# Kernel tuning notes

Measured on AMD Instinct MI355X. Metric: run time of the kernel, lower is better.

The kernel has to match this reference:

```python
import jax, jax.numpy as jnp
import numpy as np

N_NODES = 50000
N_EDGES = 625000
HIDDEN = 128
N_TYPES = 4


def setup_inputs() -> dict:
    key = jax.random.key(0)
    ks = jax.random.split(key, 10)
    s = 1.0 / np.sqrt(HIDDEN)
    return {
        "node_states": jax.random.normal(ks[0], (N_NODES, HIDDEN), dtype=jnp.float32),
        "edge_index": jax.random.randint(ks[1], (2, N_EDGES), 0, N_NODES, dtype=jnp.int64),
        "edge_type": jax.random.randint(ks[2], (N_EDGES,), 0, N_TYPES, dtype=jnp.int64),
        # per-edge-type Linear(hidden, hidden): weight [T, d, d] (torch: y = x @ W.T + b)
        "edge_W": jax.random.uniform(ks[3], (N_TYPES, HIDDEN, HIDDEN), jnp.float32, -s, s),
        "edge_b": jax.random.uniform(ks[4], (N_TYPES, HIDDEN), jnp.float32, -s, s),
        # GRUCell params (torch layout: [3d, d] for r|z|n gates)
        "w_ih": jax.random.uniform(ks[5], (3 * HIDDEN, HIDDEN), jnp.float32, -s, s),
        "w_hh": jax.random.uniform(ks[6], (3 * HIDDEN, HIDDEN), jnp.float32, -s, s),
        "b_ih": jax.random.uniform(ks[7], (3 * HIDDEN,), jnp.float32, -s, s),
        "b_hh": jax.random.uniform(ks[8], (3 * HIDDEN,), jnp.float32, -s, s),
    }


def reference(node_states, edge_index, edge_type, edge_W, edge_b, w_ih, w_hh, b_ih, b_hh):
    num_nodes = node_states.shape[0]
    src, dst = edge_index[0], edge_index[1]
    x_src = node_states[src]  # [E, d] gather of source states

    # per-edge-type linear; small fixed loop over edge types, masked accumulate
    msgs = jnp.zeros_like(x_src)
    for t in range(edge_W.shape[0]):
        m_t = x_src @ edge_W[t].T + edge_b[t]  # [E, d]
        msgs = msgs + jnp.where((edge_type == t)[:, None], m_t, 0.0)

    # scatter-sum messages into destination nodes
    agg = jax.ops.segment_sum(msgs, dst, num_segments=num_nodes)  # [N, d]

    # GRUCell(agg, node_states) — torch semantics
    gi = agg @ w_ih.T + b_ih          # [N, 3d]
    gh = node_states @ w_hh.T + b_hh  # [N, 3d]
    i_r, i_z, i_n = jnp.split(gi, 3, axis=1)
    h_r, h_z, h_n = jnp.split(gh, 3, axis=1)
    r = jax.nn.sigmoid(i_r + h_r)
    z = jax.nn.sigmoid(i_z + h_z)
    n = jnp.tanh(i_n + r * h_n)
    return (1.0 - z) * n + z * node_states
```

## Files before the change

kernel.cpp:

```cpp
#include <hip/hip_runtime.h>


typedef __attribute__((ext_vector_type(8))) short short8;
typedef __attribute__((ext_vector_type(4))) float floatx4;

#define HID 128
#define NTY 4

__device__ __forceinline__ unsigned short f2bf(float f) {
    unsigned int u = __float_as_uint(f);
    unsigned int r = (u + 0x7fffu + ((u >> 16) & 1u)) >> 16;
    return (unsigned short)r;
}
__device__ __forceinline__ float bf2f(unsigned int lo16) {
    return __uint_as_float(lo16 << 16);
}
__device__ __forceinline__ float frcp(float x) { return __builtin_amdgcn_rcpf(x); }


__global__ void prep_kernel(const float* __restrict__ h, unsigned short* __restrict__ hbf,
                            const float* __restrict__ W, unsigned short* __restrict__ Wc,
                            const float* __restrict__ w_ih, const float* __restrict__ w_hh,
                            unsigned short* __restrict__ Wg, float* __restrict__ bias4,
                            const float* __restrict__ b_ih, const float* __restrict__ b_hh,
                            int* __restrict__ deg4, int total4, int nb_cvt, int N4) {
    int b = blockIdx.x, tt = threadIdx.x;
    if (b < nb_cvt) {
        int i = b * 256 + tt;
        if (i < total4) {
            float4 v = ((const float4*)h)[i];
            uint2 o;
            o.x = (unsigned int)f2bf(v.x) | ((unsigned int)f2bf(v.y) << 16);
            o.y = (unsigned int)f2bf(v.z) | ((unsigned int)f2bf(v.w) << 16);
            ((uint2*)hbf)[i] = o;
        }
    } else if (b < nb_cvt + 256) {
        int idx = (b - nb_cvt) * 256 + tt;
        int j = idx >> 9, rem = idx & 511;
        int t = rem >> 7, k = rem & 127;
        Wc[idx] = f2bf(W[(t * HID + j) * HID + k]);
    } else if (b < nb_cvt + 768) {
        int idx = (b - nb_cvt - 256) * 256 + tt;
        int row = idx >> 8, k = idx & 255;
        int j = row >> 2, g = row & 3;
        float v = 0.0f;
        if (g == 0) v = (k < 128) ? w_ih[j * 128 + k]         : w_hh[j * 128 + (k - 128)];
        else if (g == 1) v = (k < 128) ? w_ih[(128 + j) * 128 + k] : w_hh[(128 + j) * 128 + (k - 128)];
        else if (g == 2) v = (k < 128) ? w_ih[(256 + j) * 128 + k] : 0.0f;
        else             v = (k < 128) ? 0.0f : w_hh[(256 + j) * 128 + (k - 128)];
        Wg[idx] = f2bf(v);
    } else if (b == nb_cvt + 768) {
        if (tt < 128) {
            float4 v;
            v.x = b_ih[tt] + b_hh[tt];
            v.y = b_ih[128 + tt] + b_hh[128 + tt];
            v.z = b_ih[256 + tt];
            v.w = b_hh[256 + tt];
            ((float4*)bias4)[tt] = v;
        }
    } else {
        int i = (b - nb_cvt - 769) * 256 + tt;
        if (i < N4) deg4[i] = 0;
    }
}


__global__ void hist4_kernel(const int* __restrict__ dst, const int* __restrict__ ety,
                             int* __restrict__ deg4, int E) {
    int e = blockIdx.x * blockDim.x + threadIdx.x;
    if (e < E) atomicAdd(&deg4[dst[e] * 4 + ety[e]], 1);
}

__global__ void scan_blocks4_kernel(const int* __restrict__ deg, int* __restrict__ rowptr,
                                    int* __restrict__ blocksum, int N4) {
    __shared__ int s[256];
    int t = threadIdx.x;
    int base = blockIdx.x * 1024 + t * 4;
    int v0 = 0, v1 = 0, v2 = 0, v3 = 0;
    if (base + 3 < N4) {
        v0 = deg[base]; v1 = deg[base + 1]; v2 = deg[base + 2]; v3 = deg[base + 3];
    } else {
        if (base < N4) v0 = deg[base];
        if (base + 1 < N4) v1 = deg[base + 1];
        if (base + 2 < N4) v2 = deg[base + 2];
    }
    int sum = v0 + v1 + v2 + v3;
    s[t] = sum;
    __syncthreads();
#pragma unroll
    for (int off = 1; off < 256; off <<= 1) {
        int x = (t >= off) ? s[t - off] : 0;
        __syncthreads();
        s[t] += x;
        __syncthreads();
    }
    int ex = s[t] - sum;
    if (base < N4) rowptr[base] = ex;
    if (base + 1 < N4) rowptr[base + 1] = ex + v0;
    if (base + 2 < N4) rowptr[base + 2] = ex + v0 + v1;
    if (base + 3 < N4) rowptr[base + 3] = ex + v0 + v1 + v2;
    if (t == 255) blocksum[blockIdx.x] = s[255];
}

__global__ void scan_top_kernel(const int* __restrict__ blocksum, int* __restrict__ blockoff, int nb) {
    __shared__ int s[256];
    int t = threadIdx.x;
    int v = (t < nb) ? blocksum[t] : 0;
    s[t] = v;
    __syncthreads();
#pragma unroll
    for (int off = 1; off < 256; off <<= 1) {
        int x = (t >= off) ? s[t - off] : 0;
        __syncthreads();
        s[t] += x;
        __syncthreads();
    }
    if (t < nb) blockoff[t] = s[t] - v;
}

__global__ void finalize4_kernel(int* __restrict__ rowptr, const int* __restrict__ blockoff,
                                 int* __restrict__ cursor, int N4, int E) {
    int i = blockIdx.x * blockDim.x + threadIdx.x;
    if (i >= N4) return;
    int r = rowptr[i] + blockoff[i >> 10];
    rowptr[i] = r;
    cursor[i] = r;
    if (i == 0) rowptr[N4] = E;
}

__global__ void fill4_kernel(const int* __restrict__ src, const int* __restrict__ dst,
                             const int* __restrict__ ety, int* __restrict__ cursor,
                             int* __restrict__ csr, int E) {
    int e = blockIdx.x * blockDim.x + threadIdx.x;
    if (e >= E) return;
    int pos = atomicAdd(&cursor[dst[e] * 4 + ety[e]], 1);
    csr[pos] = src[e];
}


__global__ void gather_s_kernel(const int* __restrict__ rowptr4, const int* __restrict__ csr,
                                const unsigned int* __restrict__ hbu,
                                float4* __restrict__ cnt4, unsigned int* __restrict__ Su, int N) {
    int w = blockIdx.x * (blockDim.x >> 6) + (threadIdx.x >> 6);
    if (w >= N) return;
    int lane = threadIdx.x & 63;
    int b0 = __builtin_amdgcn_readfirstlane(rowptr4[w * 4]);
    int b1 = __builtin_amdgcn_readfirstlane(rowptr4[w * 4 + 1]);
    int b2 = __builtin_amdgcn_readfirstlane(rowptr4[w * 4 + 2]);
    int b3 = __builtin_amdgcn_readfirstlane(rowptr4[w * 4 + 3]);
    int b4 = __builtin_amdgcn_readfirstlane(rowptr4[w * 4 + 4]);

    float s0 = 0.f, s1 = 0.f;
    float sn0[3], sn1[3];

    int e = b0;
    while (e + 8 <= b4) {
        int p[8];
        unsigned int u[8];
#pragma unroll
        for (int i = 0; i < 8; ++i) p[i] = csr[e + i];
#pragma unroll
        for (int i = 0; i < 8; ++i) u[i] = hbu[(size_t)p[i] * 64 + lane];
#pragma unroll
        for (int i = 0; i < 8; ++i) {
            int idx = e + i;
            if (idx == b1) { sn0[0] = s0; sn1[0] = s1; }
            if (idx == b2) { sn0[1] = s0; sn1[1] = s1; }
            if (idx == b3) { sn0[2] = s0; sn1[2] = s1; }
            s0 += bf2f(u[i] & 0xffffu);
            s1 += bf2f(u[i] >> 16);
        }
        e += 8;
    }
    {
        int rem = b4 - e;
        int p[7];
        unsigned int u[7];
#pragma unroll
        for (int i = 0; i < 7; ++i) if (i < rem) p[i] = csr[e + i];
#pragma unroll
        for (int i = 0; i < 7; ++i) if (i < rem) u[i] = hbu[(size_t)p[i] * 64 + lane];
#pragma unroll
        for (int i = 0; i < 7; ++i) {
            if (i < rem) {
                int idx = e + i;
                if (idx == b1) { sn0[0] = s0; sn1[0] = s1; }
                if (idx == b2) { sn0[1] = s0; sn1[1] = s1; }
                if (idx == b3) { sn0[2] = s0; sn1[2] = s1; }
                s0 += bf2f(u[i] & 0xffffu);
                s1 += bf2f(u[i] >> 16);
            }
        }
    }
    if (b1 == b4) { sn0[0] = s0; sn1[0] = s1; }
    if (b2 == b4) { sn0[1] = s0; sn1[1] = s1; }
    if (b3 == b4) { sn0[2] = s0; sn1[2] = s1; }

    size_t base = (size_t)w * 256 + lane;
    float a0, a1, p0 = 0.f, p1 = 0.f;
#pragma unroll
    for (int t = 0; t < 4; ++t) {
        float c0 = (t < 3) ? sn0[t] : s0;
        float c1 = (t < 3) ? sn1[t] : s1;
        a0 = c0 - p0; a1 = c1 - p1;
        p0 = c0; p1 = c1;
        Su[base + t * 64] = (unsigned int)f2bf(a0) | ((unsigned int)f2bf(a1) << 16);
    }
    if (lane == 0)
        cnt4[w] = make_float4((float)(b1 - b0), (float)(b2 - b1),
                              (float)(b3 - b2), (float)(b4 - b3));
}


__global__ __launch_bounds__(512, 4) void agg_gru(const unsigned short* __restrict__ S,
                                                  const unsigned short* __restrict__ Wc,
                                                  const unsigned short* __restrict__ Wg,
                                                  const unsigned short* __restrict__ hbf,
                                                  const float4* __restrict__ cnt4,
                                                  const float* __restrict__ eb,
                                                  const float4* __restrict__ bias4,
                                                  float* __restrict__ out, int M) {
    __shared__ __align__(16) unsigned short Sreg[64 * 128];
    __shared__ __align__(16) unsigned short Wreg[128 * 128];
    __shared__ __align__(16) unsigned short Xagg[64 * 128];
    float* OutsF = (float*)Wreg;

    const int tid = threadIdx.x;
    const int m0 = blockIdx.x * 64;
    const int lane = tid & 63, w = tid >> 6;
    const int lm = lane & 15, quad = lane >> 4;
    const uint4 Z = {0u, 0u, 0u, 0u};

    const int sr = tid >> 4;
    const int sg = tid & 15;

    floatx4 accA[4];
#pragma unroll
    for (int a = 0; a < 4; ++a) accA[a] = (floatx4){0.f, 0.f, 0.f, 0.f};

#pragma unroll 1
    for (int c = 0; c < 4; ++c) {
        {
            int gA = m0 + sr, gB = m0 + 32 + sr;
            uint4 vA = (gA < M) ? *(const uint4*)(S + (size_t)gA * 512 + c * 128 + sg * 8) : Z;
            uint4 vB = (gB < M) ? *(const uint4*)(S + (size_t)gB * 512 + c * 128 + sg * 8) : Z;
            *(uint4*)&Sreg[sr * 128 + ((sg ^ (sr & 7)) << 3)] = vA;
            *(uint4*)&Sreg[(32 + sr) * 128 + ((sg ^ (sr & 7)) << 3)] = vB;
        }
#pragma unroll
        for (int p = 0; p < 4; ++p) {
            int j = p * 32 + sr;
            uint4 v = *(const uint4*)(Wc + (size_t)j * 512 + c * 128 + sg * 8);
            *(uint4*)&Wreg[j * 128 + ((sg ^ (j & 7)) << 3)] = v;
        }
        __syncthreads();
#pragma unroll
        for (int ss = 0; ss < 4; ++ss) {
            int g = ss * 4 + quad;
            short8 bw = *(const short8*)&Wreg[(w * 16 + lm) * 128 + ((g ^ (lm & 7)) << 3)];
#pragma unroll
            for (int mi = 0; mi < 4; ++mi) {
                short8 av = *(const short8*)&Sreg[(mi * 16 + lm) * 128 + ((g ^ (lm & 7)) << 3)];
                accA[mi] = __builtin_amdgcn_mfma_f32_16x16x32_bf16(av, bw, accA[mi], 0, 0, 0);
            }
        }
        __syncthreads();
    }

    {
        int j = w * 16 + lm;
        float e0 = eb[j], e1 = eb[HID + j], e2 = eb[2 * HID + j], e3 = eb[3 * HID + j];
        int jg = j >> 3, jr = j & 7;
#pragma unroll
        for (int mi = 0; mi < 4; ++mi) {
#pragma unroll
            for (int r = 0; r < 4; ++r) {
                int nl = mi * 16 + quad * 4 + r;
                int gn = m0 + nl;
                if (gn >= M) gn = M - 1;
                float4 c4 = cnt4[gn];
                float v = accA[mi][r] + c4.x * e0 + c4.y * e1 + c4.z * e2 + c4.w * e3;
                Xagg[nl * 128 + ((jg ^ (nl & 7)) << 3) + jr] = f2bf(v);
            }
        }
    }
    __syncthreads();

    {
        int gA = m0 + sr, gB = m0 + 32 + sr;
        uint4 vA = (gA < M) ? *(const uint4*)(hbf + (size_t)gA * HID + sg * 8) : Z;
        uint4 vB = (gB < M) ? *(const uint4*)(hbf + (size_t)gB * HID + sg * 8) : Z;
        *(uint4*)&Sreg[sr * 128 + ((sg ^ (sr & 7)) << 3)] = vA;
        *(uint4*)&Sreg[(32 + sr) * 128 + ((sg ^ (sr & 7)) << 3)] = vB;
    }

    float fin[4][4];

#pragma unroll 1
    for (int gc = 0; gc < 4; ++gc) {
        floatx4 accB[4];
#pragma unroll
        for (int a = 0; a < 4; ++a) accB[a] = (floatx4){0.f, 0.f, 0.f, 0.f};

#pragma unroll 1
        for (int kc = 0; kc < 2; ++kc) {
#pragma unroll
            for (int p = 0; p < 4; ++p) {
                int rr = p * 32 + sr;
                int grow = gc * 128 + rr;
                uint4 v = *(const uint4*)(Wg + (size_t)grow * 256 + kc * 128 + sg * 8);
                *(uint4*)&Wreg[rr * 128 + ((sg ^ (rr & 7)) << 3)] = v;
            }
            __syncthreads();
#pragma unroll
            for (int ss = 0; ss < 4; ++ss) {
                int g = ss * 4 + quad;
                short8 af = *(const short8*)&Wreg[(w * 16 + lm) * 128 + ((g ^ (lm & 7)) << 3)];
#pragma unroll
                for (int ni = 0; ni < 4; ++ni) {
                    const unsigned short* bsrc = kc ? Sreg : Xagg;
                    short8 bfr = *(const short8*)&bsrc[(ni * 16 + lm) * 128 + ((g ^ (lm & 7)) << 3)];
                    accB[ni] = __builtin_amdgcn_mfma_f32_16x16x32_bf16(af, bfr, accB[ni], 0, 0, 0);
                }
            }
            __syncthreads();
        }

        {
            int j = gc * 32 + w * 4 + quad;
            float4 bb = bias4[j];
            int jg = j >> 3, jr = j & 7;
#pragma unroll
            for (int ni = 0; ni < 4; ++ni) {
                int nl = ni * 16 + lm;
                float g0 = accB[ni][0], g1 = accB[ni][1];
                float g2 = accB[ni][2], g3 = accB[ni][3];
                float rr = frcp(1.f + __expf(-(g0 + bb.x)));
                float zz = frcp(1.f + __expf(-(g1 + bb.y)));
                float aa = g2 + bb.z + rr * (g3 + bb.w);
                float nn = 1.f - 2.f * frcp(1.f + __expf(2.f * aa));
                float hv = bf2f((unsigned int)Sreg[nl * 128 + ((jg ^ (nl & 7)) << 3) + jr]);
                fin[gc][ni] = nn + zz * (hv - nn);
            }
        }
    }
    __syncthreads();

#pragma unroll
    for (int gc = 0; gc < 4; ++gc) {
        int j = gc * 32 + w * 4 + quad;
        int gq = j >> 2, jr = j & 3;
#pragma unroll
        for (int ni = 0; ni < 4; ++ni) {
            int nl = ni * 16 + lm;
            OutsF[nl * 128 + ((gq ^ (nl & 7)) << 2) + jr] = fin[gc][ni];
        }
    }
    __syncthreads();

    {
        int row = tid >> 3;
        int cb = (tid & 7) * 16;
        int node = m0 + row;
        if (node < M) {
            float* dstp = out + (size_t)node * HID + cb;
#pragma unroll
            for (int i = 0; i < 4; ++i) {
                int gq = (cb >> 2) + i;
                *(float4*)(dstp + i * 4) = *(const float4*)&OutsF[row * 128 + ((gq ^ (row & 7)) << 2)];
            }
        }
    }
}


extern "C" void kernel_launch(void* const* d_in, const int* in_sizes, int n_in,
                              void* d_out, int out_size, void* d_ws, size_t ws_size,
                              hipStream_t stream) {
    const float* node_states = (const float*)d_in[0];
    const int*   edge_index  = (const int*)d_in[1];
    const int*   edge_type   = (const int*)d_in[2];
    const float* edge_W      = (const float*)d_in[3];
    const float* edge_b      = (const float*)d_in[4];
    const float* w_ih        = (const float*)d_in[5];
    const float* w_hh        = (const float*)d_in[6];
    const float* b_ih        = (const float*)d_in[7];
    const float* b_hh        = (const float*)d_in[8];

    const int M = in_sizes[0] / HID;
    const int E = in_sizes[1] / 2;
    const int N4 = M * 4;
    const int* src = edge_index;
    const int* dst = edge_index + E;

    char* ws = (char*)d_ws;
    size_t off = 0;
    unsigned short* hbf   = (unsigned short*)(ws + off); off += (size_t)M * HID * 2;
    float*          bias4 = (float*)(ws + off);          off += (size_t)128 * 4 * 4;
    unsigned short* S     = (unsigned short*)(ws + off); off += (size_t)M * 512 * 2;
    unsigned short* Wcat  = (unsigned short*)(ws + off); off += (size_t)128 * 512 * 2;
    unsigned short* Wgru  = (unsigned short*)(ws + off); off += (size_t)512 * 256 * 2;
    float*          cnt4  = (float*)(ws + off);          off += (size_t)M * 4 * 4;
    int* deg4     = (int*)(ws + off); off += (size_t)N4 * 4;
    int* rowptr4  = (int*)(ws + off); off += (size_t)(N4 + 1) * 4;
    int* cursor4  = (int*)(ws + off); off += (size_t)N4 * 4;
    int* blocksum = (int*)(ws + off); off += 256 * 4;
    int* blockoff = (int*)(ws + off); off += 256 * 4;
    int* csr      = (int*)(ws + off); off += (size_t)E * 4;

    const int total4 = M * HID / 4;
    const int nb_cvt = (total4 + 255) / 256;
    const int nb_zero = (N4 + 255) / 256;
    const int nb_scan = (N4 + 1023) / 1024;

    prep_kernel<<<nb_cvt + 769 + nb_zero, 256, 0, stream>>>(
        node_states, hbf, edge_W, Wcat, w_ih, w_hh, Wgru, bias4, b_ih, b_hh,
        deg4, total4, nb_cvt, N4);

    hist4_kernel<<<(E + 255) / 256, 256, 0, stream>>>(dst, edge_type, deg4, E);
    scan_blocks4_kernel<<<nb_scan, 256, 0, stream>>>(deg4, rowptr4, blocksum, N4);
    scan_top_kernel<<<1, 256, 0, stream>>>(blocksum, blockoff, nb_scan);
    finalize4_kernel<<<(N4 + 255) / 256, 256, 0, stream>>>(rowptr4, blockoff, cursor4, N4, E);
    fill4_kernel<<<(E + 255) / 256, 256, 0, stream>>>(src, dst, edge_type, cursor4, csr, E);

    gather_s_kernel<<<(M + 3) / 4, 256, 0, stream>>>(rowptr4, csr, (const unsigned int*)hbf,
                                                     (float4*)cnt4, (unsigned int*)S, M);

    agg_gru<<<(M + 63) / 64, 512, 0, stream>>>(S, Wcat, Wgru, hbf, (const float4*)cnt4,
                                               edge_b, (const float4*)bias4, (float*)d_out, M);
}
```

Measured before the change: 244.6 us.

## Fuse CSR build into one cooperative kernel; double-buffer agg_gru weight tiles

New measurement: 819.8 us. 235% more time.

```diff
diff --git a/kernel.cpp b/kernel.cpp
--- a/kernel.cpp
+++ b/kernel.cpp
@@ -1,4 +1,7 @@
 #include <hip/hip_runtime.h>
+#include <hip/hip_cooperative_groups.h>
+
+namespace cg = cooperative_groups;
 
 
 typedef __attribute__((ext_vector_type(8))) short short8;
@@ -23,7 +26,7 @@
                             const float* __restrict__ w_ih, const float* __restrict__ w_hh,
                             unsigned short* __restrict__ Wg, float* __restrict__ bias4,
                             const float* __restrict__ b_ih, const float* __restrict__ b_hh,
-                            int* __restrict__ deg4, int total4, int nb_cvt, int N4) {
+                            int total4, int nb_cvt) {
     int b = blockIdx.x, tt = threadIdx.x;
     if (b < nb_cvt) {
         int i = b * 256 + tt;
@@ -49,7 +52,7 @@
         else if (g == 2) v = (k < 128) ? w_ih[(256 + j) * 128 + k] : 0.0f;
         else             v = (k < 128) ? 0.0f : w_hh[(256 + j) * 128 + (k - 128)];
         Wg[idx] = f2bf(v);
-    } else if (b == nb_cvt + 768) {
+    } else {
         if (tt < 128) {
             float4 v;
             v.x = b_ih[tt] + b_hh[tt];
@@ -58,83 +61,88 @@
             v.w = b_hh[256 + tt];
             ((float4*)bias4)[tt] = v;
         }
-    } else {
-        int i = (b - nb_cvt - 769) * 256 + tt;
-        if (i < N4) deg4[i] = 0;
-    }
-}
-
-
-__global__ void hist4_kernel(const int* __restrict__ dst, const int* __restrict__ ety,
-                             int* __restrict__ deg4, int E) {
-    int e = blockIdx.x * blockDim.x + threadIdx.x;
-    if (e < E) atomicAdd(&deg4[dst[e] * 4 + ety[e]], 1);
-}
-
-__global__ void scan_blocks4_kernel(const int* __restrict__ deg, int* __restrict__ rowptr,
-                                    int* __restrict__ blocksum, int N4) {
+    }
+}
+
+
+struct CsrArgs {
+    const int* src; const int* dst; const int* ety;
+    int* deg4; int* rowptr4; int* cursor4; int* blocksum; int* blockoff; int* csr;
+    int E, N4;
+};
+
+__global__ __launch_bounds__(256, 4) void csr_build(CsrArgs a) {
+    cg::grid_group grid = cg::this_grid();
     __shared__ int s[256];
-    int t = threadIdx.x;
-    int base = blockIdx.x * 1024 + t * 4;
-    int v0 = 0, v1 = 0, v2 = 0, v3 = 0;
-    if (base + 3 < N4) {
-        v0 = deg[base]; v1 = deg[base + 1]; v2 = deg[base + 2]; v3 = deg[base + 3];
-    } else {
-        if (base < N4) v0 = deg[base];
-        if (base + 1 < N4) v1 = deg[base + 1];
-        if (base + 2 < N4) v2 = deg[base + 2];
-    }
-    int sum = v0 + v1 + v2 + v3;
-    s[t] = sum;
-    __syncthreads();
-#pragma unroll
-    for (int off = 1; off < 256; off <<= 1) {
-        int x = (t >= off) ? s[t - off] : 0;
+    const int t = threadIdx.x;
+    const int gtid = blockIdx.x * 256 + t;
+    const int nth = gridDim.x * 256;
+
+    for (int i = gtid; i < a.N4; i += nth) a.deg4[i] = 0;
+    grid.sync();
+
+    for (int e = gtid; e < a.E; e += nth)
+        atomicAdd(&a.deg4[a.dst[e] * 4 + a.ety[e]], 1);
+    grid.sync();
+
+    const int nbscan = (a.N4 + 1023) >> 10;
+    for (int vb = blockIdx.x; vb < nbscan; vb += gridDim.x) {
+        int base = vb * 1024 + t * 4;
+        int v0 = 0, v1 = 0, v2 = 0, v3 = 0;
+        if (base + 3 < a.N4) {
+            v0 = a.deg4[base]; v1 = a.deg4[base + 1]; v2 = a.deg4[base + 2]; v3 = a.deg4[base + 3];
+        } else {
+            if (base < a.N4) v0 = a.deg4[base];
+            if (base + 1 < a.N4) v1 = a.deg4[base + 1];
+            if (base + 2 < a.N4) v2 = a.deg4[base + 2];
+        }
+        int sum = v0 + v1 + v2 + v3;
+        s[t] = sum;
         __syncthreads();
-        s[t] += x;
+#pragma unroll
+        for (int off = 1; off < 256; off <<= 1) {
+            int x = (t >= off) ? s[t - off] : 0;
+            __syncthreads();
+            s[t] += x;
+            __syncthreads();
+        }
+        int ex = s[t] - sum;
+        if (base < a.N4) a.rowptr4[base] = ex;
+        if (base + 1 < a.N4) a.rowptr4[base + 1] = ex + v0;
+        if (base + 2 < a.N4) a.rowptr4[base + 2] = ex + v0 + v1;
+        if (base + 3 < a.N4) a.rowptr4[base + 3] = ex + v0 + v1 + v2;
+        if (t == 255) a.blocksum[vb] = s[255];
         __syncthreads();
     }
-    int ex = s[t] - sum;
-    if (base < N4) rowptr[base] = ex;
-    if (base + 1 < N4) rowptr[base + 1] = ex + v0;
-    if (base + 2 < N4) rowptr[base + 2] = ex + v0 + v1;
-    if (base + 3 < N4) rowptr[base + 3] = ex + v0 + v1 + v2;
-    if (t == 255) blocksum[blockIdx.x] = s[255];
-}
-
-__global__ void scan_top_kernel(const int* __restrict__ blocksum, int* __restrict__ blockoff, int nb) {
-    __shared__ int s[256];
-    int t = threadIdx.x;
-    int v = (t < nb) ? blocksum[t] : 0;
-    s[t] = v;
-    __syncthreads();
-#pragma unroll
-    for (int off = 1; off < 256; off <<= 1) {
-        int x = (t >= off) ? s[t - off] : 0;
+    grid.sync();
+
+    if (blockIdx.x == 0) {
+        int v = (t < nbscan) ? a.blocksum[t] : 0;
+        s[t] = v;
         __syncthreads();
-        s[t] += x;
-        __syncthreads();
-    }
-    if (t < nb) blockoff[t] = s[t] - v;
-}
-
-__global__ void finalize4_kernel(int* __restrict__ rowptr, const int* __restrict__ blockoff,
-                                 int* __restrict__ cursor, int N4, int E) {
-    int i = blockIdx.x * blockDim.x + threadIdx.x;
-    if (i >= N4) return;
-    int r = rowptr[i] + blockoff[i >> 10];
-    rowptr[i] = r;
-    cursor[i] = r;
-    if (i == 0) rowptr[N4] = E;
-}
-
-__global__ void fill4_kernel(const int* __restrict__ src, const int* __restrict__ dst,
-                             const int* __restrict__ ety, int* __restrict__ cursor,
-                             int* __restrict__ csr, int E) {
-    int e = blockIdx.x * blockDim.x + threadIdx.x;
-    if (e >= E) return;
-    int pos = atomicAdd(&cursor[dst[e] * 4 + ety[e]], 1);
-    csr[pos] = src[e];
+#pragma unroll
+        for (int off = 1; off < 256; off <<= 1) {
+            int x = (t >= off) ? s[t - off] : 0;
+            __syncthreads();
+            s[t] += x;
+            __syncthreads();
+        }
+        if (t < nbscan) a.blockoff[t] = s[t] - v;
+    }
+    grid.sync();
+
+    for (int i = gtid; i < a.N4; i += nth) {
+        int r = a.rowptr4[i] + a.blockoff[i >> 10];
+        a.rowptr4[i] = r;
+        a.cursor4[i] = r;
+    }
+    if (gtid == 0) a.rowptr4[a.N4] = a.E;
+    grid.sync();
+
+    for (int e = gtid; e < a.E; e += nth) {
+        int pos = atomicAdd(&a.cursor4[a.dst[e] * 4 + a.ety[e]], 1);
+        a.csr[pos] = a.src[e];
+    }
 }
 
 
@@ -220,51 +228,55 @@
                                                   const float* __restrict__ eb,
                                                   const float4* __restrict__ bias4,
                                                   float* __restrict__ out, int M) {
-    __shared__ __align__(16) unsigned short Sreg[64 * 128];
-    __shared__ __align__(16) unsigned short Wreg[128 * 128];
-    __shared__ __align__(16) unsigned short Xagg[64 * 128];
-    float* OutsF = (float*)Wreg;
+    __shared__ __align__(16) unsigned char smem[65536];
+    unsigned short* SdB = (unsigned short*)smem;
+    unsigned short* WdB = (unsigned short*)(smem + 16384);
+    unsigned short* Xag = (unsigned short*)(smem + 49152);
+    unsigned short* Hbt = (unsigned short*)smem;
+    float* OutsF = (float*)smem;
 
     const int tid = threadIdx.x;
     const int m0 = blockIdx.x * 64;
     const int lane = tid & 63, w = tid >> 6;
     const int lm = lane & 15, quad = lane >> 4;
-    const uint4 Z = {0u, 0u, 0u, 0u};
-
-    const int sr = tid >> 4;
-    const int sg = tid & 15;
+
+    const int sr = tid >> 3;
+    const int g8 = tid & 7;
+    const int srow = (m0 + sr < M) ? (m0 + sr) : (M - 1);
 
     floatx4 accA[4];
 #pragma unroll
     for (int a = 0; a < 4; ++a) accA[a] = (floatx4){0.f, 0.f, 0.f, 0.f};
 
+    uint4 sv  = *(const uint4*)(S + (size_t)srow * 512 + g8 * 8);
+    uint4 wv0 = *(const uint4*)(Wc + (size_t)sr * 512 + g8 * 8);
+    uint4 wv1 = *(const uint4*)(Wc + (size_t)(64 + sr) * 512 + g8 * 8);
+
 #pragma unroll 1
-    for (int c = 0; c < 4; ++c) {
-        {
-            int gA = m0 + sr, gB = m0 + 32 + sr;
-            uint4 vA = (gA < M) ? *(const uint4*)(S + (size_t)gA * 512 + c * 128 + sg * 8) : Z;
-            uint4 vB = (gB < M) ? *(const uint4*)(S + (size_t)gB * 512 + c * 128 + sg * 8) : Z;
-            *(uint4*)&Sreg[sr * 128 + ((sg ^ (sr & 7)) << 3)] = vA;
-            *(uint4*)&Sreg[(32 + sr) * 128 + ((sg ^ (sr & 7)) << 3)] = vB;
-        }
-#pragma unroll
-        for (int p = 0; p < 4; ++p) {
-            int j = p * 32 + sr;
-            uint4 v = *(const uint4*)(Wc + (size_t)j * 512 + c * 128 + sg * 8);
-            *(uint4*)&Wreg[j * 128 + ((sg ^ (j & 7)) << 3)] = v;
-        }
+    for (int c = 0; c < 8; ++c) {
+        uint4 sn, wn0, wn1;
+        if (c < 7) {
+            sn  = *(const uint4*)(S + (size_t)srow * 512 + (c + 1) * 64 + g8 * 8);
+            wn0 = *(const uint4*)(Wc + (size_t)sr * 512 + (c + 1) * 64 + g8 * 8);
+            wn1 = *(const uint4*)(Wc + (size_t)(64 + sr) * 512 + (c + 1) * 64 + g8 * 8);
+        }
+        unsigned short* Sp = SdB + (c & 1) * 4096;
+        unsigned short* Wp = WdB + (c & 1) * 8192;
+        *(uint4*)&Sp[sr * 64 + ((g8 ^ (sr & 7)) << 3)] = sv;
+        *(uint4*)&Wp[sr * 64 + ((g8 ^ (sr & 7)) << 3)] = wv0;
+        *(uint4*)&Wp[(64 + sr) * 64 + ((g8 ^ (sr & 7)) << 3)] = wv1;
         __syncthreads();
 #pragma unroll
-        for (int ss = 0; ss < 4; ++ss) {
-            int g = ss * 4 + quad;
-            short8 bw = *(const short8*)&Wreg[(w * 16 + lm) * 128 + ((g ^ (lm & 7)) << 3)];
+        for (int ks = 0; ks < 2; ++ks) {
+            int g = ks * 4 + quad;
+            short8 bw = *(const short8*)&Wp[(w * 16 + lm) * 64 + ((g ^ (lm & 7)) << 3)];
 #pragma unroll
             for (int mi = 0; mi < 4; ++mi) {
-                short8 av = *(const short8*)&Sreg[(mi * 16 + lm) * 128 + ((g ^ (lm & 7)) << 3)];
+                short8 av = *(const short8*)&Sp[(mi * 16 + lm) * 64 + ((g ^ (lm & 7)) << 3)];
                 accA[mi] = __builtin_amdgcn_mfma_f32_16x16x32_bf16(av, bw, accA[mi], 0, 0, 0);
             }
         }
-        __syncthreads();
+        sv = sn; wv0 = wn0; wv1 = wn1;
     }
 
     {
@@ -280,53 +292,63 @@
                 if (gn >= M) gn = M - 1;
                 float4 c4 = cnt4[gn];
                 float v = accA[mi][r] + c4.x * e0 + c4.y * e1 + c4.z * e2 + c4.w * e3;
-                Xagg[nl * 128 + ((jg ^ (nl & 7)) << 3) + jr] = f2bf(v);
+                Xag[nl * 128 + ((jg ^ (nl & 7)) << 3) + jr] = f2bf(v);
             }
         }
     }
     __syncthreads();
 
     {
-        int gA = m0 + sr, gB = m0 + 32 + sr;
-        uint4 vA = (gA < M) ? *(const uint4*)(hbf + (size_t)gA * HID + sg * 8) : Z;
-        uint4 vB = (gB < M) ? *(const uint4*)(hbf + (size_t)gB * HID + sg * 8) : Z;
-        *(uint4*)&Sreg[sr * 128 + ((sg ^ (sr & 7)) << 3)] = vA;
-        *(uint4*)&Sreg[(32 + sr) * 128 + ((sg ^ (sr & 7)) << 3)] = vB;
-    }
-
+        int hr = tid >> 4, sg = tid & 15;
+        int ga = (m0 + hr < M) ? (m0 + hr) : (M - 1);
+        int gb = (m0 + 32 + hr < M) ? (m0 + 32 + hr) : (M - 1);
+        uint4 va = *(const uint4*)(hbf + (size_t)ga * HID + sg * 8);
+        uint4 vb = *(const uint4*)(hbf + (size_t)gb * HID + sg * 8);
+        *(uint4*)&Hbt[hr * 128 + ((sg ^ (hr & 7)) << 3)] = va;
+        *(uint4*)&Hbt[(32 + hr) * 128 + ((sg ^ ((32 + hr) & 7)) << 3)] = vb;
+    }
+
+    uint4 w0 = *(const uint4*)(Wg + (size_t)sr * 256 + g8 * 8);
+    uint4 w1 = *(const uint4*)(Wg + (size_t)(64 + sr) * 256 + g8 * 8);
+
+    floatx4 accB[4];
     float fin[4][4];
 
 #pragma unroll 1
-    for (int gc = 0; gc < 4; ++gc) {
-        floatx4 accB[4];
-#pragma unroll
-        for (int a = 0; a < 4; ++a) accB[a] = (floatx4){0.f, 0.f, 0.f, 0.f};
-
-#pragma unroll 1
-        for (int kc = 0; kc < 2; ++kc) {
-#pragma unroll
-            for (int p = 0; p < 4; ++p) {
-                int rr = p * 32 + sr;
-                int grow = gc * 128 + rr;
-                uint4 v = *(const uint4*)(Wg + (size_t)grow * 256 + kc * 128 + sg * 8);
-                *(uint4*)&Wreg[rr * 128 + ((sg ^ (rr & 7)) << 3)] = v;
-            }
-            __syncthreads();
-#pragma unroll
-            for (int ss = 0; ss < 4; ++ss) {
-                int g = ss * 4 + quad;
-                short8 af = *(const short8*)&Wreg[(w * 16 + lm) * 128 + ((g ^ (lm & 7)) << 3)];
-#pragma unroll
-                for (int ni = 0; ni < 4; ++ni) {
-                    const unsigned short* bsrc = kc ? Sreg : Xagg;
-                    short8 bfr = *(const short8*)&bsrc[(ni * 16 + lm) * 128 + ((g ^ (lm & 7)) << 3)];
-                    accB[ni] = __builtin_amdgcn_mfma_f32_16x16x32_bf16(af, bfr, accB[ni], 0, 0, 0);
-                }
-            }
-            __syncthreads();
-        }
-
-        {
+    for (int s = 0; s < 16; ++s) {
+        int gc = s >> 2, kc = s & 3;
+        uint4 n0, n1;
+        if (s < 15) {
+            int s1i = s + 1;
+            int gcn = s1i >> 2, kcn = s1i & 3;
+            const unsigned short* base = Wg + (size_t)(gcn * 128) * 256 + kcn * 64;
+            n0 = *(const uint4*)(base + (size_t)sr * 256 + g8 * 8);
+            n1 = *(const uint4*)(base + (size_t)(64 + sr) * 256 + g8 * 8);
+        }
+        unsigned short* Wp = WdB + (s & 1) * 8192;
+        *(uint4*)&Wp[sr * 64 + ((g8 ^ (sr & 7)) << 3)] = w0;
+        *(uint4*)&Wp[(64 + sr) * 64 + ((g8 ^ (sr & 7)) << 3)] = w1;
+        __syncthreads();
+
+        if (kc == 0) {
+#pragma unroll
+            for (int a = 0; a < 4; ++a) accB[a] = (floatx4){0.f, 0.f, 0.f, 0.f};
+        }
+        const unsigned short* Bsrc = (kc < 2) ? Xag : Hbt;
+        const int kb = (kc & 1) * 8;
+#pragma unroll
+        for (int ks = 0; ks < 2; ++ks) {
+            int g = ks * 4 + quad;
+            short8 af = *(const short8*)&Wp[(w * 16 + lm) * 64 + ((g ^ (lm & 7)) << 3)];
+            int G = kb + g;
+#pragma unroll
+            for (int ni = 0; ni < 4; ++ni) {
+                int nl = ni * 16 + lm;
+                short8 bfr = *(const short8*)&Bsrc[nl * 128 + ((G ^ (nl & 7)) << 3)];
+                accB[ni] = __builtin_amdgcn_mfma_f32_16x16x32_bf16(af, bfr, accB[ni], 0, 0, 0);
+            }
+        }
+        if (kc == 3) {
             int j = gc * 32 + w * 4 + quad;
             float4 bb = bias4[j];
             int jg = j >> 3, jr = j & 7;
@@ -339,10 +361,11 @@
                 float zz = frcp(1.f + __expf(-(g1 + bb.y)));
                 float aa = g2 + bb.z + rr * (g3 + bb.w);
                 float nn = 1.f - 2.f * frcp(1.f + __expf(2.f * aa));
-                float hv = bf2f((unsigned int)Sreg[nl * 128 + ((jg ^ (nl & 7)) << 3) + jr]);
+                float hv = bf2f((unsigned int)Hbt[nl * 128 + ((jg ^ (nl & 7)) << 3) + jr]);
                 fin[gc][ni] = nn + zz * (hv - nn);
             }
         }
+        w0 = n0; w1 = n1;
     }
     __syncthreads();
 
@@ -410,18 +433,19 @@
 
     const int total4 = M * HID / 4;
     const int nb_cvt = (total4 + 255) / 256;
-    const int nb_zero = (N4 + 255) / 256;
-    const int nb_scan = (N4 + 1023) / 1024;
-
-    prep_kernel<<<nb_cvt + 769 + nb_zero, 256, 0, stream>>>(
+
+    prep_kernel<<<nb_cvt + 769, 256, 0, stream>>>(
         node_states, hbf, edge_W, Wcat, w_ih, w_hh, Wgru, bias4, b_ih, b_hh,
-        deg4, total4, nb_cvt, N4);
-
-    hist4_kernel<<<(E + 255) / 256, 256, 0, stream>>>(dst, edge_type, deg4, E);
-    scan_blocks4_kernel<<<nb_scan, 256, 0, stream>>>(deg4, rowptr4, blocksum, N4);
-    scan_top_kernel<<<1, 256, 0, stream>>>(blocksum, blockoff, nb_scan);
-    finalize4_kernel<<<(N4 + 255) / 256, 256, 0, stream>>>(rowptr4, blockoff, cursor4, N4, E);
-    fill4_kernel<<<(E + 255) / 256, 256, 0, stream>>>(src, dst, edge_type, cursor4, csr, E);
+        total4, nb_cvt);
+
+    CsrArgs ca;
+    ca.src = src; ca.dst = dst; ca.ety = edge_type;
+    ca.deg4 = deg4; ca.rowptr4 = rowptr4; ca.cursor4 = cursor4;
+    ca.blocksum = blocksum; ca.blockoff = blockoff; ca.csr = csr;
+    ca.E = E; ca.N4 = N4;
+    void* params[] = {&ca};
+    hipLaunchCooperativeKernel((void*)csr_build, dim3(1024), dim3(256),
+                               params, 0, stream);
 
     gather_s_kernel<<<(M + 3) / 4, 256, 0, stream>>>(rowptr4, csr, (const unsigned int*)hbf,
                                                      (float4*)cnt4, (unsigned int*)S, M);
```

## Shrink agg_gru tile to 32 nodes with 256 threads and 2x2 MFMA tiles

Applied to the files above, without the earlier changes.

New measurement: 245.9 us. About the same (+0.5%).

```diff
diff --git a/kernel.cpp b/kernel.cpp
--- a/kernel.cpp
+++ b/kernel.cpp
@@ -212,7 +212,7 @@
 }
 
 
-__global__ __launch_bounds__(512, 4) void agg_gru(const unsigned short* __restrict__ S,
+__global__ __launch_bounds__(256, 3) void agg_gru(const unsigned short* __restrict__ S,
                                                   const unsigned short* __restrict__ Wc,
                                                   const unsigned short* __restrict__ Wg,
                                                   const unsigned short* __restrict__ hbf,
@@ -220,36 +220,40 @@
                                                   const float* __restrict__ eb,
                                                   const float4* __restrict__ bias4,
                                                   float* __restrict__ out, int M) {
-    __shared__ __align__(16) unsigned short Sreg[64 * 128];
-    __shared__ __align__(16) unsigned short Wreg[128 * 128];
-    __shared__ __align__(16) unsigned short Xagg[64 * 128];
-    float* OutsF = (float*)Wreg;
+    __shared__ __align__(16) unsigned char smem[49152];
+    unsigned short* Sreg = (unsigned short*)smem;
+    unsigned short* Hbt  = (unsigned short*)(smem + 8192);
+    unsigned short* Wreg = (unsigned short*)(smem + 16384);
+    unsigned short* Xag  = Sreg;
+    float* OutsF = (float*)(smem + 16384);
 
     const int tid = threadIdx.x;
-    const int m0 = blockIdx.x * 64;
+    const int m0 = blockIdx.x * 32;
     const int lane = tid & 63, w = tid >> 6;
     const int lm = lane & 15, quad = lane >> 4;
-    const uint4 Z = {0u, 0u, 0u, 0u};
-
-    const int sr = tid >> 4;
+
+    const int hr = tid >> 4;
     const int sg = tid & 15;
-
-    floatx4 accA[4];
-#pragma unroll
-    for (int a = 0; a < 4; ++a) accA[a] = (floatx4){0.f, 0.f, 0.f, 0.f};
+    const int gA = (m0 + hr < M) ? (m0 + hr) : (M - 1);
+    const int gB = (m0 + 16 + hr < M) ? (m0 + 16 + hr) : (M - 1);
+
+    floatx4 accA[2][2];
+#pragma unroll
+    for (int x = 0; x < 2; ++x)
+#pragma unroll
+        for (int y = 0; y < 2; ++y) accA[x][y] = (floatx4){0.f, 0.f, 0.f, 0.f};
 
 #pragma unroll 1
     for (int c = 0; c < 4; ++c) {
         {
-            int gA = m0 + sr, gB = m0 + 32 + sr;
-            uint4 vA = (gA < M) ? *(const uint4*)(S + (size_t)gA * 512 + c * 128 + sg * 8) : Z;
-            uint4 vB = (gB < M) ? *(const uint4*)(S + (size_t)gB * 512 + c * 128 + sg * 8) : Z;
-            *(uint4*)&Sreg[sr * 128 + ((sg ^ (sr & 7)) << 3)] = vA;
-            *(uint4*)&Sreg[(32 + sr) * 128 + ((sg ^ (sr & 7)) << 3)] = vB;
-        }
-#pragma unroll
-        for (int p = 0; p < 4; ++p) {
-            int j = p * 32 + sr;
+            uint4 vA = *(const uint4*)(S + (size_t)gA * 512 + c * 128 + sg * 8);
+            uint4 vB = *(const uint4*)(S + (size_t)gB * 512 + c * 128 + sg * 8);
+            *(uint4*)&Sreg[hr * 128 + ((sg ^ (hr & 7)) << 3)] = vA;
+            *(uint4*)&Sreg[(16 + hr) * 128 + ((sg ^ (hr & 7)) << 3)] = vB;
+        }
+#pragma unroll
+        for (int p = 0; p < 8; ++p) {
+            int j = p * 16 + hr;
             uint4 v = *(const uint4*)(Wc + (size_t)j * 512 + c * 128 + sg * 8);
             *(uint4*)&Wreg[j * 128 + ((sg ^ (j & 7)) << 3)] = v;
         }
@@ -257,90 +261,106 @@
 #pragma unroll
         for (int ss = 0; ss < 4; ++ss) {
             int g = ss * 4 + quad;
-            short8 bw = *(const short8*)&Wreg[(w * 16 + lm) * 128 + ((g ^ (lm & 7)) << 3)];
-#pragma unroll
-            for (int mi = 0; mi < 4; ++mi) {
-                short8 av = *(const short8*)&Sreg[(mi * 16 + lm) * 128 + ((g ^ (lm & 7)) << 3)];
-                accA[mi] = __builtin_amdgcn_mfma_f32_16x16x32_bf16(av, bw, accA[mi], 0, 0, 0);
-            }
+            short8 av[2], bw[2];
+#pragma unroll
+            for (int mi = 0; mi < 2; ++mi)
+                av[mi] = *(const short8*)&Sreg[(mi * 16 + lm) * 128 + ((g ^ (lm & 7)) << 3)];
+#pragma unroll
+            for (int ni = 0; ni < 2; ++ni)
+                bw[ni] = *(const short8*)&Wreg[(w * 32 + ni * 16 + lm) * 128 + ((g ^ (lm & 7)) << 3)];
+#pragma unroll
+            for (int mi = 0; mi < 2; ++mi)
+#pragma unroll
+                for (int ni = 0; ni < 2; ++ni)
+                    accA[mi][ni] = __builtin_amdgcn_mfma_f32_16x16x32_bf16(av[mi], bw[ni], accA[mi][ni], 0, 0, 0);
         }
         __syncthreads();
     }
 
     {
-        int j = w * 16 + lm;
-        float e0 = eb[j], e1 = eb[HID + j], e2 = eb[2 * HID + j], e3 = eb[3 * HID + j];
-        int jg = j >> 3, jr = j & 7;
-#pragma unroll
-        for (int mi = 0; mi < 4; ++mi) {
-#pragma unroll
-            for (int r = 0; r < 4; ++r) {
-                int nl = mi * 16 + quad * 4 + r;
-                int gn = m0 + nl;
-                if (gn >= M) gn = M - 1;
-                float4 c4 = cnt4[gn];
-                float v = accA[mi][r] + c4.x * e0 + c4.y * e1 + c4.z * e2 + c4.w * e3;
-                Xagg[nl * 128 + ((jg ^ (nl & 7)) << 3) + jr] = f2bf(v);
+        uint4 vA = *(const uint4*)(hbf + (size_t)gA * HID + sg * 8);
+        uint4 vB = *(const uint4*)(hbf + (size_t)gB * HID + sg * 8);
+        *(uint4*)&Hbt[hr * 128 + ((sg ^ (hr & 7)) << 3)] = vA;
+        *(uint4*)&Hbt[(16 + hr) * 128 + ((sg ^ (hr & 7)) << 3)] = vB;
+    }
+
+    {
+#pragma unroll
+        for (int ni = 0; ni < 2; ++ni) {
+            int j = w * 32 + ni * 16 + lm;
+            float e0 = eb[j], e1 = eb[HID + j], e2 = eb[2 * HID + j], e3 = eb[3 * HID + j];
+            int jg = j >> 3, jr = j & 7;
+#pragma unroll
+            for (int mi = 0; mi < 2; ++mi) {
+#pragma unroll
+                for (int r = 0; r < 4; ++r) {
+                    int nl = mi * 16 + quad * 4 + r;
+                    int gn = m0 + nl;
+                    if (gn >= M) gn = M - 1;
+                    float4 c4 = cnt4[gn];
+                    float v = accA[mi][ni][r] + c4.x * e0 + c4.y * e1 + c4.z * e2 + c4.w * e3;
+                    Xag[nl * 128 + ((jg ^ (nl & 7)) << 3) + jr] = f2bf(v);
+                }
             }
         }
     }
     __syncthreads();
 
-    {
-        int gA = m0 + sr, gB = m0 + 32 + sr;
-        uint4 vA = (gA < M) ? *(const uint4*)(hbf + (size_t)gA * HID + sg * 8) : Z;
-        uint4 vB = (gB < M) ? *(const uint4*)(hbf + (size_t)gB * HID + sg * 8) : Z;
-        *(uint4*)&Sreg[sr * 128 + ((sg ^ (sr & 7)) << 3)] = vA;
-        *(uint4*)&Sreg[(32 + sr) * 128 + ((sg ^ (sr & 7)) << 3)] = vB;
-    }
-
-    float fin[4][4];
+    float fin[4][2][2];
 
 #pragma unroll 1
     for (int gc = 0; gc < 4; ++gc) {
-        floatx4 accB[4];
-#pragma unroll
-        for (int a = 0; a < 4; ++a) accB[a] = (floatx4){0.f, 0.f, 0.f, 0.f};
+        floatx4 acc2[2][2];
+#pragma unroll
+        for (int x = 0; x < 2; ++x)
+#pragma unroll
+            for (int y = 0; y < 2; ++y) acc2[x][y] = (floatx4){0.f, 0.f, 0.f, 0.f};
 
 #pragma unroll 1
         for (int kc = 0; kc < 2; ++kc) {
 #pragma unroll
-            for (int p = 0; p < 4; ++p) {
-                int rr = p * 32 + sr;
-                int grow = gc * 128 + rr;
-                uint4 v = *(const uint4*)(Wg + (size_t)grow * 256 + kc * 128 + sg * 8);
+            for (int p = 0; p < 8; ++p) {
+                int rr = p * 16 + hr;
+                uint4 v = *(const uint4*)(Wg + (size_t)(gc * 128 + rr) * 256 + kc * 128 + sg * 8);
                 *(uint4*)&Wreg[rr * 128 + ((sg ^ (rr & 7)) << 3)] = v;
             }
             __syncthreads();
+            const unsigned short* Bsrc = kc ? Hbt : Xag;
 #pragma unroll
             for (int ss = 0; ss < 4; ++ss) {
                 int g = ss * 4 + quad;
-                short8 af = *(const short8*)&Wreg[(w * 16 + lm) * 128 + ((g ^ (lm & 7)) << 3)];
-#pragma unroll
-                for (int ni = 0; ni < 4; ++ni) {
-                    const unsigned short* bsrc = kc ? Sreg : Xagg;
-                    short8 bfr = *(const short8*)&bsrc[(ni * 16 + lm) * 128 + ((g ^ (lm & 7)) << 3)];
-                    accB[ni] = __builtin_amdgcn_mfma_f32_16x16x32_bf16(af, bfr, accB[ni], 0, 0, 0);
-                }
+                short8 af[2], bfr[2];
+#pragma unroll
+                for (int mi2 = 0; mi2 < 2; ++mi2)
+                    af[mi2] = *(const short8*)&Wreg[(w * 32 + mi2 * 16 + lm) * 128 + ((g ^ (lm & 7)) << 3)];
+#pragma unroll
+                for (int ni = 0; ni < 2; ++ni)
+                    bfr[ni] = *(const short8*)&Bsrc[(ni * 16 + lm) * 128 + ((g ^ (lm & 7)) << 3)];
+#pragma unroll
+                for (int mi2 = 0; mi2 < 2; ++mi2)
+#pragma unroll
+                    for (int ni = 0; ni < 2; ++ni)
+                        acc2[mi2][ni] = __builtin_amdgcn_mfma_f32_16x16x32_bf16(af[mi2], bfr[ni], acc2[mi2][ni], 0, 0, 0);
             }
             __syncthreads();
         }
 
-        {
-            int j = gc * 32 + w * 4 + quad;
+#pragma unroll
+        for (int mi2 = 0; mi2 < 2; ++mi2) {
+            int j = gc * 32 + w * 8 + mi2 * 4 + quad;
             float4 bb = bias4[j];
             int jg = j >> 3, jr = j & 7;
 #pragma unroll
-            for (int ni = 0; ni < 4; ++ni) {
+            for (int ni = 0; ni < 2; ++ni) {
                 int nl = ni * 16 + lm;
-                float g0 = accB[ni][0], g1 = accB[ni][1];
-                float g2 = accB[ni][2], g3 = accB[ni][3];
+                float g0 = acc2[mi2][ni][0], g1 = acc2[mi2][ni][1];
+                float g2 = acc2[mi2][ni][2], g3 = acc2[mi2][ni][3];
                 float rr = frcp(1.f + __expf(-(g0 + bb.x)));
                 float zz = frcp(1.f + __expf(-(g1 + bb.y)));
                 float aa = g2 + bb.z + rr * (g3 + bb.w);
                 float nn = 1.f - 2.f * frcp(1.f + __expf(2.f * aa));
-                float hv = bf2f((unsigned int)Sreg[nl * 128 + ((jg ^ (nl & 7)) << 3) + jr]);
-                fin[gc][ni] = nn + zz * (hv - nn);
+                float hv = bf2f((unsigned int)Hbt[nl * 128 + ((jg ^ (nl & 7)) << 3) + jr]);
+                fin[gc][mi2][ni] = nn + zz * (hv - nn);
             }
         }
     }
@@ -348,12 +368,15 @@
 
 #pragma unroll
     for (int gc = 0; gc < 4; ++gc) {
-        int j = gc * 32 + w * 4 + quad;
-        int gq = j >> 2, jr = j & 3;
-#pragma unroll
-        for (int ni = 0; ni < 4; ++ni) {
-            int nl = ni * 16 + lm;
-            OutsF[nl * 128 + ((gq ^ (nl & 7)) << 2) + jr] = fin[gc][ni];
+#pragma unroll
+        for (int mi2 = 0; mi2 < 2; ++mi2) {
+            int j = gc * 32 + w * 8 + mi2 * 4 + quad;
+            int gq = j >> 2, jr = j & 3;
+#pragma unroll
+            for (int ni = 0; ni < 2; ++ni) {
+                int nl = ni * 16 + lm;
+                OutsF[nl * 128 + ((gq ^ (nl & 7)) << 2) + jr] = fin[gc][mi2][ni];
+            }
         }
     }
     __syncthreads();
@@ -426,6 +449,6 @@
     gather_s_kernel<<<(M + 3) / 4, 256, 0, stream>>>(rowptr4, csr, (const unsigned int*)hbf,
                                                      (float4*)cnt4, (unsigned int*)S, M);
 
-    agg_gru<<<(M + 63) / 64, 512, 0, stream>>>(S, Wcat, Wgru, hbf, (const float4*)cnt4,
+    agg_gru<<<(M + 31) / 32, 256, 0, stream>>>(S, Wcat, Wgru, hbf, (const float4*)cnt4,
                                                edge_b, (const float4*)bias4, (float*)d_out, M);
 }
```
